# Performance work log

Measured on AMD Instinct MI355X. Metric: run time of the kernel, lower is better.

## Reference

```python
import jax, jax.numpy as jnp
import numpy as np

V, D, N = 100000, 64, 16


def setup_inputs() -> dict:
    key = jax.random.key(0)
    k = jax.random.split(key, 7)
    return {
        "x": jax.random.normal(k[0], (V, D), dtype=jnp.float32),
        "state": jax.random.normal(k[1], (V, D, N), dtype=jnp.float32),
        "log_nA": jax.random.uniform(k[2], (D, N), dtype=jnp.float32),
        "B": jax.random.normal(k[3], (D, N), dtype=jnp.float32),
        "C": jax.random.normal(k[4], (D, N, N), dtype=jnp.float32) * (1.0 / np.sqrt(N)),
        "w_delta": jax.random.normal(k[5], (1, D), dtype=jnp.float32) * 0.02,
        "b_delta": jax.random.uniform(k[6], (1,), dtype=jnp.float32),
    }


def reference(x, state, log_nA, B, C, w_delta, b_delta):
    # delta = Softplus(Linear(x)) -> [V]
    delta = jax.nn.softplus(x @ w_delta.T + b_delta)[:, 0]  # [V]
    A = -jnp.exp(log_nA)                                    # [D, N]
    # ZOH discretization, broadcast over nodes: [V, D, N]
    A_zoh = jnp.exp(delta[:, None, None] * A[None])
    B_x = (delta[:, None, None] * B[None]) * x[:, :, None]  # [V, D, N]
    new_state = A_zoh * state + B_x                         # [V, D, N]
    # per-feature small contraction with C: v d n, d n q -> v d q
    return jnp.einsum('vdn,dnq->vdq', new_state, C)
```

## Files before the change

### kernel.cpp

```cpp
#include <hip/hip_runtime.h>


constexpr int D = 64;
constexpr int N = 16;
constexpr int VPW = 16;
constexpr int CD = 8;
constexpr int NCHUNK = D / CD;
constexpr int NS_STRIDE = CD * N + 4;

__global__ __launch_bounds__(256, 4)
void siso_kernel(const float* __restrict__ x,
                 const float* __restrict__ state,
                 const float* __restrict__ log_nA,
                 const float* __restrict__ Bm,
                 const float* __restrict__ Cm,
                 const float* __restrict__ w_delta,
                 const float* __restrict__ b_delta,
                 float* __restrict__ out,
                 int V)
{
    __shared__ __align__(16) float ns_lds[4][VPW * NS_STRIDE];

    const int tid  = threadIdx.x;
    const int wave = tid >> 6;
    const int lane = tid & 63;
    float* nsw = ns_lds[wave];

    const int vbase = blockIdx.x * (4 * VPW) + wave * VPW;

    const int vv0 = lane >> 2;
    const int kk  = lane & 3;
    const int v0  = vbase + vv0;
    float z = 0.f;
    if (v0 < V) {
        const float4* xr = (const float4*)(x + (size_t)v0 * D) + kk * 4;
        const float4* wr = (const float4*)(w_delta) + kk * 4;
#pragma unroll
        for (int c = 0; c < 4; ++c) {
            float4 xv = xr[c];
            float4 wv = wr[c];
            z += xv.x * wv.x + xv.y * wv.y + xv.z * wv.z + xv.w * wv.w;
        }
    }
    z += __shfl_xor(z, 1, 64);
    z += __shfl_xor(z, 2, 64);
    z += b_delta[0];
    const float delta0 = (z > 20.f) ? z : __logf(1.f + __expf(z));

    const int qg = lane & 3;
    const int vv = lane >> 2;
    const int v2 = vbase + vv;

    for (int dc = 0; dc < NCHUNK; ++dc) {
        const int dbase = dc * CD;

#pragma unroll
        for (int j = 0; j < 8; ++j) {
            const int voff   = 2 * j + (lane >> 5);
            const int within = (j * 64 + lane) & 31;
            const int v      = vbase + voff;
            const int doff   = within >> 2;
            const int d      = dbase + doff;
            const int f4n    = within & 3;

            float4 s = make_float4(0.f, 0.f, 0.f, 0.f);
            float xv = 0.f;
            if (v < V) {
                s  = ((const float4*)(state + (size_t)v * (D * N) + dbase * N))[within];
                xv = x[(size_t)v * D + d];
            }
            const float4 ga = ((const float4*)log_nA)[d * 4 + f4n];
            const float4 gb = ((const float4*)Bm)[d * 4 + f4n];
            const float dl  = __shfl(delta0, voff * 4, 64);
            const float dx  = dl * xv;
            float4 ns;
            ns.x = __expf(-dl * __expf(ga.x)) * s.x + dx * gb.x;
            ns.y = __expf(-dl * __expf(ga.y)) * s.y + dx * gb.y;
            ns.z = __expf(-dl * __expf(ga.z)) * s.z + dx * gb.z;
            ns.w = __expf(-dl * __expf(ga.w)) * s.w + dx * gb.w;
            *(float4*)(nsw + voff * NS_STRIDE + within * 4) = ns;
        }
        __syncthreads();

        if (v2 < V) {
            const float* nsv = nsw + vv * NS_STRIDE;
            for (int doff = 0; doff < CD; ++doff) {
                const int d = dbase + doff;
                const float* Crow = Cm + (size_t)d * (N * N) + qg * 4;
                const float* nsd  = nsv + doff * N;
                float4 acc = make_float4(0.f, 0.f, 0.f, 0.f);
#pragma unroll
                for (int n = 0; n < N; ++n) {
                    const float  a  = nsd[n];
                    const float4 c4 = *(const float4*)(Crow + n * N);
                    acc.x += a * c4.x;
                    acc.y += a * c4.y;
                    acc.z += a * c4.z;
                    acc.w += a * c4.w;
                }
                *(float4*)(out + (size_t)v2 * (D * N) + d * N + qg * 4) = acc;
            }
        }
        __syncthreads();
    }
}

extern "C" void kernel_launch(void* const* d_in, const int* in_sizes, int n_in,
                              void* d_out, int out_size, void* d_ws, size_t ws_size,
                              hipStream_t stream) {
    const float* x       = (const float*)d_in[0];
    const float* state   = (const float*)d_in[1];
    const float* log_nA  = (const float*)d_in[2];
    const float* Bm      = (const float*)d_in[3];
    const float* Cm      = (const float*)d_in[4];
    const float* w_delta = (const float*)d_in[5];
    const float* b_delta = (const float*)d_in[6];
    float* out = (float*)d_out;

    const int V = in_sizes[0] / D;
    const int blocks = (V + 4 * VPW - 1) / (4 * VPW);

    siso_kernel<<<blocks, 256, 0, stream>>>(x, state, log_nA, Bm, Cm,
                                            w_delta, b_delta, out, V);
}
```

Measured before the change: 950.5 us.

## Replace block barriers with wave-local LDS waits and shrink chunks and blocks

Each wave uses only its own LDS slice, so the block-wide barriers are replaced with a wave-level lgkmcnt wait plus a compiler memory fence. Blocks shrink to two waves and the feature chunk to four, with a higher occupancy hint. Per-lane delta shuffles and exp(log_nA) are hoisted out of the inner loop, and the C contraction reads the new state as float4 from LDS. The kernel is memory-bound on streaming state and out, so these compute and sync savings may matter little. It relies on wave-synchronous execution for LDS visibility.

```diff
diff --git a/kernel.cpp b/kernel.cpp
--- a/kernel.cpp
+++ b/kernel.cpp
@@ -4,11 +4,12 @@
 constexpr int D = 64;
 constexpr int N = 16;
 constexpr int VPW = 16;
-constexpr int CD = 8;
+constexpr int WPB = 2;
+constexpr int CD  = 4;
 constexpr int NCHUNK = D / CD;
 constexpr int NS_STRIDE = CD * N + 4;
 
-__global__ __launch_bounds__(256, 4)
+__global__ __launch_bounds__(WPB * 64, 8)
 void siso_kernel(const float* __restrict__ x,
                  const float* __restrict__ state,
                  const float* __restrict__ log_nA,
@@ -19,14 +20,14 @@
                  float* __restrict__ out,
                  int V)
 {
-    __shared__ __align__(16) float ns_lds[4][VPW * NS_STRIDE];
+    __shared__ __align__(16) float ns_lds[WPB][VPW * NS_STRIDE];
 
     const int tid  = threadIdx.x;
     const int wave = tid >> 6;
     const int lane = tid & 63;
     float* nsw = ns_lds[wave];
 
-    const int vbase = blockIdx.x * (4 * VPW) + wave * VPW;
+    const int vbase = blockIdx.x * (WPB * VPW) + wave * VPW;
 
     const int vv0 = lane >> 2;
     const int kk  = lane & 3;
@@ -47,61 +48,71 @@
     z += b_delta[0];
     const float delta0 = (z > 20.f) ? z : __logf(1.f + __expf(z));
 
-    const int qg = lane & 3;
-    const int vv = lane >> 2;
-    const int v2 = vbase + vv;
+    const int within = lane & 15;
+    const int vsub   = lane >> 4;
+    const int doffl  = within >> 2;
+    const int qg     = lane & 3;
+    const int vv     = lane >> 2;
+    const int v2     = vbase + vv;
+
+    float dl[4];
+#pragma unroll
+    for (int j = 0; j < 4; ++j)
+        dl[j] = __shfl(delta0, (j * 4 + vsub) * 4, 64);
 
     for (int dc = 0; dc < NCHUNK; ++dc) {
         const int dbase = dc * CD;
 
+        const float4 ga = ((const float4*)log_nA)[dbase * 4 + within];
+        const float4 gb = ((const float4*)Bm)[dbase * 4 + within];
+        float4 na;
+        na.x = __expf(ga.x); na.y = __expf(ga.y);
+        na.z = __expf(ga.z); na.w = __expf(ga.w);
+
 #pragma unroll
-        for (int j = 0; j < 8; ++j) {
-            const int voff   = 2 * j + (lane >> 5);
-            const int within = (j * 64 + lane) & 31;
-            const int v      = vbase + voff;
-            const int doff   = within >> 2;
-            const int d      = dbase + doff;
-            const int f4n    = within & 3;
-
+        for (int j = 0; j < 4; ++j) {
+            const int voff = j * 4 + vsub;
+            const int v    = vbase + voff;
             float4 s = make_float4(0.f, 0.f, 0.f, 0.f);
-            float xv = 0.f;
+            float  xv = 0.f;
             if (v < V) {
-                s  = ((const float4*)(state + (size_t)v * (D * N) + dbase * N))[within];
-                xv = x[(size_t)v * D + d];
+                s  = ((const float4*)(state + (size_t)v * (D * N)))[dbase * 4 + within];
+                xv = x[(size_t)v * D + dbase + doffl];
             }
-            const float4 ga = ((const float4*)log_nA)[d * 4 + f4n];
-            const float4 gb = ((const float4*)Bm)[d * 4 + f4n];
-            const float dl  = __shfl(delta0, voff * 4, 64);
-            const float dx  = dl * xv;
+            const float dj = dl[j];
+            const float dx = dj * xv;
             float4 ns;
-            ns.x = __expf(-dl * __expf(ga.x)) * s.x + dx * gb.x;
-            ns.y = __expf(-dl * __expf(ga.y)) * s.y + dx * gb.y;
-            ns.z = __expf(-dl * __expf(ga.z)) * s.z + dx * gb.z;
-            ns.w = __expf(-dl * __expf(ga.w)) * s.w + dx * gb.w;
+            ns.x = __expf(-dj * na.x) * s.x + dx * gb.x;
+            ns.y = __expf(-dj * na.y) * s.y + dx * gb.y;
+            ns.z = __expf(-dj * na.z) * s.z + dx * gb.z;
+            ns.w = __expf(-dj * na.w) * s.w + dx * gb.w;
             *(float4*)(nsw + voff * NS_STRIDE + within * 4) = ns;
         }
-        __syncthreads();
+        asm volatile("s_waitcnt lgkmcnt(0)" ::: "memory");
 
         if (v2 < V) {
-            const float* nsv = nsw + vv * NS_STRIDE;
+            const float4* nsq = (const float4*)(nsw + vv * NS_STRIDE);
+#pragma unroll
             for (int doff = 0; doff < CD; ++doff) {
                 const int d = dbase + doff;
                 const float* Crow = Cm + (size_t)d * (N * N) + qg * 4;
-                const float* nsd  = nsv + doff * N;
                 float4 acc = make_float4(0.f, 0.f, 0.f, 0.f);
 #pragma unroll
-                for (int n = 0; n < N; ++n) {
-                    const float  a  = nsd[n];
-                    const float4 c4 = *(const float4*)(Crow + n * N);
-                    acc.x += a * c4.x;
-                    acc.y += a * c4.y;
-                    acc.z += a * c4.z;
-                    acc.w += a * c4.w;
+                for (int n4 = 0; n4 < 4; ++n4) {
+                    const float4 a  = nsq[doff * 4 + n4];
+                    const float4 c0 = *(const float4*)(Crow + (n4 * 4 + 0) * N);
+                    const float4 c1 = *(const float4*)(Crow + (n4 * 4 + 1) * N);
+                    const float4 c2 = *(const float4*)(Crow + (n4 * 4 + 2) * N);
+                    const float4 c3 = *(const float4*)(Crow + (n4 * 4 + 3) * N);
+                    acc.x += a.x * c0.x + a.y * c1.x + a.z * c2.x + a.w * c3.x;
+                    acc.y += a.x * c0.y + a.y * c1.y + a.z * c2.y + a.w * c3.y;
+                    acc.z += a.x * c0.z + a.y * c1.z + a.z * c2.z + a.w * c3.z;
+                    acc.w += a.x * c0.w + a.y * c1.w + a.z * c2.w + a.w * c3.w;
                 }
                 *(float4*)(out + (size_t)v2 * (D * N) + d * N + qg * 4) = acc;
             }
         }
-        __syncthreads();
+        asm volatile("" ::: "memory");
     }
 }
 
@@ -118,8 +129,8 @@
     float* out = (float*)d_out;
 
     const int V = in_sizes[0] / D;
-    const int blocks = (V + 4 * VPW - 1) / (4 * VPW);
+    const int blocks = (V + WPB * VPW - 1) / (WPB * VPW);
 
-    siso_kernel<<<blocks, 256, 0, stream>>>(x, state, log_nA, Bm, Cm,
-                                            w_delta, b_delta, out, V);
+    siso_kernel<<<blocks, WPB * 64, 0, stream>>>(x, state, log_nA, Bm, Cm,
+                                                 w_delta, b_delta, out, V);
 }
```

Result: slower. 1.038 ms (+9.3%).
